# Optimization experiments

Hardware: AMD Instinct MI355X
Metric: run time of the kernel (lower is better)

The kernel has to match this reference:

```python
import jax, jax.numpy as jnp
import numpy as np
from jax import lax

B, CHI, CHO, H, W = 4, 256, 256, 96, 96
K = 9  # 3x3 kernel taps
BN_EPS = 1e-5


def setup_inputs() -> dict:
    key = jax.random.key(0)
    k1, k2, k3 = jax.random.split(key, 3)
    x = jax.random.normal(k1, (B, CHI, H, W), dtype=jnp.float32)
    # offset/mask conv: zero-init in DCNv2; use small random so sampling is exercised
    w_offset = jax.random.normal(k2, (3 * K, CHI, 3, 3), dtype=jnp.float32) * 0.01
    b_offset = jnp.zeros((3 * K,), dtype=jnp.float32)
    fan_in = CHI * K
    w_conv = jax.random.normal(k3, (CHO, CHI, 3, 3), dtype=jnp.float32) / np.sqrt(fan_in)
    b_conv = jnp.zeros((CHO,), dtype=jnp.float32)
    gamma = jnp.ones((CHO,), dtype=jnp.float32)
    beta = jnp.zeros((CHO,), dtype=jnp.float32)
    return {"x": x, "w_offset": w_offset, "b_offset": b_offset,
            "w_conv": w_conv, "b_conv": b_conv, "gamma": gamma, "beta": beta}


def _bilinear_gather(img, py, px):
    # img: [C, H, W]; py, px: [K, H, W] float sampling positions (zero padding)
    Hin, Win = img.shape[1], img.shape[2]
    y0 = jnp.floor(py)
    x0 = jnp.floor(px)
    ly = py - y0  # fractional parts (differentiable w.r.t. offsets)
    lx = px - x0
    y0i = y0.astype(jnp.int32)
    x0i = x0.astype(jnp.int32)

    def corner(yi, xi, wgt):
        valid = (yi >= 0) & (yi < Hin) & (xi >= 0) & (xi < Win)
        yc = jnp.clip(yi, 0, Hin - 1)
        xc = jnp.clip(xi, 0, Win - 1)
        v = img[:, yc, xc]  # [C, K, H, W]
        return v * (wgt * valid.astype(wgt.dtype))[None]

    return (corner(y0i, x0i, (1 - ly) * (1 - lx))
            + corner(y0i, x0i + 1, (1 - ly) * lx)
            + corner(y0i + 1, x0i, ly * (1 - lx))
            + corner(y0i + 1, x0i + 1, ly * lx))


def _forward(x, w_offset, b_offset, w_conv, b_conv, gamma, beta):
    # offset/mask branch: plain 3x3 conv, pad 1, stride 1
    om = lax.conv_general_dilated(
        x, w_offset, window_strides=(1, 1), padding=((1, 1), (1, 1)),
        dimension_numbers=("NCHW", "OIHW", "NCHW"))
    om = om + b_offset[None, :, None, None]            # [B, 27, H, W]
    dy = om[:, 0:2 * K:2]                              # [B, 9, H, W]
    dx = om[:, 1:2 * K:2]                              # [B, 9, H, W]
    mask = jax.nn.sigmoid(om[:, 2 * K:])               # [B, 9, H, W]

    # base sampling grid: p0 + pn  (stride 1, pad 1, dilation 1)
    ky, kx = jnp.meshgrid(jnp.arange(3), jnp.arange(3), indexing="ij")
    ky = ky.reshape(K).astype(x.dtype)
    kx = kx.reshape(K).astype(x.dtype)
    hh = jnp.arange(x.shape[2], dtype=x.dtype)
    ww = jnp.arange(x.shape[3], dtype=x.dtype)
    py = dy + (hh[None, :, None] + ky[:, None, None] - 1.0)[None]  # [B,9,H,W]
    px = dx + (ww[None, None, :] + kx[:, None, None] - 1.0)[None]  # [B,9,H,W]

    cols = jax.vmap(_bilinear_gather)(x, py, px)       # [B, C, 9, H, W]
    cols = cols * mask[:, None]                        # modulated (DCNv2)

    wk = w_conv.reshape(w_conv.shape[0], w_conv.shape[1], K)
    out = jnp.einsum("bckhw,ock->bohw", cols, wk) + b_conv[None, :, None, None]

    # BatchNorm2d (training mode: batch stats) + ReLU
    mu = out.mean(axis=(0, 2, 3))
    var = out.var(axis=(0, 2, 3))
    xh = (out - mu[None, :, None, None]) * lax.rsqrt(var + BN_EPS)[None, :, None, None]
    y = gamma[None, :, None, None] * xh + beta[None, :, None, None]
    return jax.nn.relu(y)


def reference(x, w_offset, b_offset, w_conv, b_conv, gamma, beta):
    return _forward(x, w_offset, b_offset, w_conv, b_conv, gamma, beta)
```

## Files before the change

### kernel.cpp

```cpp
#include <hip/hip_runtime.h>
#include <math.h>

#define BN_    4
#define CHI_   256
#define CHO_   256
#define HH_    96
#define WW_    96
#define HW_    (HH_*WW_)
#define KK_    9
#define CK_    (CHI_*KK_)
#define NRED_  (BN_*HW_)
#define BN_EPS_ 1e-5f


typedef short short8 __attribute__((ext_vector_type(8)));
typedef float f32x4  __attribute__((ext_vector_type(4)));

__device__ __forceinline__ unsigned short f2bf(float v) {
    union { float f; unsigned u; } c; c.f = v;
    unsigned lsb = (c.u >> 16) & 1u;
    c.u += 0x7fffu + lsb;
    return (unsigned short)(c.u >> 16);
}

__global__ __launch_bounds__(256) void w2b_perm(
    const float* __restrict__ w, unsigned short* __restrict__ wb)
{
    int idx = blockIdx.x * 256 + threadIdx.x;
    int o  = idx / CK_;
    int kk = idx - o * CK_;
    int k  = kk >> 8;
    int c  = kk & 255;
    wb[idx] = f2bf(w[o * CK_ + c * KK_ + k]);
}

__global__ __launch_bounds__(256) void w2b_perm27(
    const float* __restrict__ w, unsigned short* __restrict__ wb)
{
    int idx = blockIdx.x * 256 + threadIdx.x;
    int o  = idx / CK_;
    int kk = idx - o * CK_;
    int k  = kk >> 8;
    int c  = kk & 255;
    wb[idx] = f2bf(w[o * CK_ + c * KK_ + k]);
}

__global__ __launch_bounds__(256) void transpose_x(
    const float* __restrict__ x, float* __restrict__ xt)
{
    __shared__ float tile[64][65];
    const int t = threadIdx.x;
    const int bid = blockIdx.x;
    const int b  = bid / (144 * 4);
    const int r  = bid - b * 576;
    const int pt = r >> 2, ct = r & 3;
    const int p0 = pt * 64, c0 = ct * 64;

    const int px = t & 63, g = t >> 6;
#pragma unroll
    for (int i = 0; i < 16; i++) {
        int cr = g + i * 4;
        tile[cr][px] = x[((size_t)b * CHI_ + c0 + cr) * HW_ + p0 + px];
    }
    __syncthreads();
    const int c = t & 63;
#pragma unroll
    for (int i = 0; i < 16; i++) {
        int pr = g + i * 4;
        xt[((size_t)b * HW_ + p0 + pr) * CHI_ + c0 + c] = tile[c][pr];
    }
}

__global__ __launch_bounds__(256) void offset_nhwc(
    const float* __restrict__ xt, const unsigned short* __restrict__ wob,
    const float* __restrict__ bo, float* __restrict__ om)
{
    __shared__ __align__(16) unsigned short sW[32 * 64];
    __shared__ __align__(16) unsigned short sB[64 * 64];

    const int t = threadIdx.x;
    const int bid = blockIdx.x;
    const int u   = (bid & 7) * 72 + (bid >> 3);
    const int pixtile = u % 144;
    const int b       = u / 144;
    const int p0 = pixtile * 64;

    const int lane = t & 63, wave = t >> 6;
    const int quad = lane >> 4, l15 = lane & 15;
    const int pxl  = t >> 2;
    const int cg   = t & 3;
    const int aro  = t >> 3;
    const int ako  = t & 7;

    f32x4 acc[2];
    acc[0] = (f32x4){0.f,0.f,0.f,0.f};
    acc[1] = (f32x4){0.f,0.f,0.f,0.f};

    const float* xtb = xt + (size_t)b * HW_ * CHI_;
    char* sWb = (char*)sW;
    char* sBb = (char*)sB;

    const int p = p0 + pxl;
    const int h = p / WW_, w = p % WW_;

    for (int kc = 0; kc < 36; kc++) {
        if (kc) __syncthreads();
        {
            uint4 v = make_uint4(0u, 0u, 0u, 0u);
            if (aro < 27)
                v = *reinterpret_cast<const uint4*>(
                    wob + (size_t)aro * CK_ + kc * 64 + ako * 8);
            *reinterpret_cast<uint4*>(
                sWb + (aro << 7) + ((ako << 4) ^ ((aro & 7) << 4))) = v;
        }
        {
            const int k  = kc >> 2;
            const int c0 = (kc & 3) << 6;
            const int yy = h + k / 3 - 1;
            const int xx = w + (k % 3) - 1;
            const bool ok = ((unsigned)yy < HH_) & ((unsigned)xx < WW_);
            union { unsigned short s[16]; uint4 q[2]; } pk;
            if (ok) {
                const float4* src = reinterpret_cast<const float4*>(
                    xtb + (size_t)(yy * WW_ + xx) * CHI_ + c0 + cg * 16);
#pragma unroll
                for (int i = 0; i < 4; i++) {
                    float4 f = src[i];
                    pk.s[i * 4 + 0] = f2bf(f.x);
                    pk.s[i * 4 + 1] = f2bf(f.y);
                    pk.s[i * 4 + 2] = f2bf(f.z);
                    pk.s[i * 4 + 3] = f2bf(f.w);
                }
            } else {
                pk.q[0] = make_uint4(0u, 0u, 0u, 0u);
                pk.q[1] = make_uint4(0u, 0u, 0u, 0u);
            }
            const int u0 = cg << 1;
            *reinterpret_cast<uint4*>(
                sBb + (pxl << 7) + ((u0 << 4) ^ ((pxl & 7) << 4))) = pk.q[0];
            *reinterpret_cast<uint4*>(
                sBb + (pxl << 7) + (((u0 + 1) << 4) ^ ((pxl & 7) << 4))) = pk.q[1];
        }
        __syncthreads();
#pragma unroll
        for (int ks = 0; ks < 2; ks++) {
            short8 a0, a1, b0;
            {
                int r = l15;
                a0 = *reinterpret_cast<const short8*>(
                    sWb + (r << 7) + (((ks << 6) + (quad << 4)) ^ ((r & 7) << 4)));
                r = 16 + l15;
                a1 = *reinterpret_cast<const short8*>(
                    sWb + (r << 7) + (((ks << 6) + (quad << 4)) ^ ((r & 7) << 4)));
                r = wave * 16 + l15;
                b0 = *reinterpret_cast<const short8*>(
                    sBb + (r << 7) + (((ks << 6) + (quad << 4)) ^ ((r & 7) << 4)));
            }
            acc[0] = __builtin_amdgcn_mfma_f32_16x16x32_bf16(a0, b0, acc[0], 0, 0, 0);
            acc[1] = __builtin_amdgcn_mfma_f32_16x16x32_bf16(a1, b0, acc[1], 0, 0, 0);
        }
    }

#pragma unroll
    for (int mt = 0; mt < 2; mt++) {
#pragma unroll
        for (int r = 0; r < 4; r++) {
            int oc = mt * 16 + quad * 4 + r;
            if (oc < 27) {
                int pix = p0 + wave * 16 + l15;
                om[((size_t)b * 27 + oc) * HW_ + pix] = acc[mt][r] + bo[oc];
            }
        }
    }
}

__global__ __launch_bounds__(256, 4) void deform_fused(
    const float* __restrict__ xt, const float* __restrict__ om,
    const unsigned short* __restrict__ wb, const float* __restrict__ bconv,
    float* __restrict__ outb)
{
    __shared__ __align__(16) unsigned short sA[CHO_ * 64];
    __shared__ __align__(16) unsigned short sB[32 * 64];
    __shared__ float s_py[KK_ * 32], s_px[KK_ * 32], s_mask[KK_ * 32];

    const int t = threadIdx.x;
    const int bid = blockIdx.x;
    const int u   = (bid & 7) * 144 + (bid >> 3);
    const int pixtile = u % 288;
    const int b       = u / 288;
    const int p0 = pixtile * 32;

    for (int e = t; e < KK_ * 32; e += 256) {
        int k = e >> 5, i = e & 31;
        int p = p0 + i;
        int h = p / WW_, w = p % WW_;
        const float* omb = om + ((size_t)b * 27) * HW_ + p;
        float dy = omb[(2 * k) * HW_];
        float dx = omb[(2 * k + 1) * HW_];
        float m  = omb[(18 + k) * HW_];
        s_py[e]   = dy + (float)(h + k / 3 - 1);
        s_px[e]   = dx + (float)(w + (k % 3) - 1);
        s_mask[e] = 1.f / (1.f + __expf(-m));
    }

    const int lane = t & 63, wave = t >> 6;
    const int quad = lane >> 4, l15 = lane & 15;
    const int pxl  = t >> 3;
    const int cg   = t & 7;

    f32x4 acc[4][2];
#pragma unroll
    for (int m = 0; m < 4; m++)
#pragma unroll
        for (int n = 0; n < 2; n++)
            acc[m][n] = (f32x4){0.f, 0.f, 0.f, 0.f};

    const float* xtb = xt + (size_t)b * HW_ * CHI_;
    char* sAb = (char*)sA;
    char* sBb = (char*)sB;

    __syncthreads();

    for (int kc = 0; kc < 36; kc++) {
        const int j0 = kc * 64;
        if (kc) __syncthreads();
#pragma unroll
        for (int n = 0; n < 8; n++) {
            int e = t + n * 256;
            int ocl = e >> 3, ko = e & 7;
            uint4 v = *reinterpret_cast<const uint4*>(
                wb + (size_t)ocl * CK_ + j0 + ko * 8);
            *reinterpret_cast<uint4*>(
                sAb + (ocl << 7) + ((ko << 4) ^ ((ocl & 7) << 4))) = v;
        }
        {
            const int k  = kc >> 2;
            const int c0 = (kc & 3) << 6;
            const int e  = k * 32 + pxl;
            float py = s_py[e], pxx = s_px[e], msk = s_mask[e];
            float y0f = floorf(py), x0f = floorf(pxx);
            float ly = py - y0f, lx = pxx - x0f;
            int y0 = (int)y0f, x0 = (int)x0f;
            float vy0 = ((unsigned)y0       < HH_) ? 1.f : 0.f;
            float vy1 = ((unsigned)(y0 + 1) < HH_) ? 1.f : 0.f;
            float vx0 = ((unsigned)x0       < WW_) ? 1.f : 0.f;
            float vx1 = ((unsigned)(x0 + 1) < WW_) ? 1.f : 0.f;
            int yc0 = min(max(y0, 0), HH_ - 1), yc1 = min(max(y0 + 1, 0), HH_ - 1);
            int xc0 = min(max(x0, 0), WW_ - 1), xc1 = min(max(x0 + 1, 0), WW_ - 1);
            float wy0 = 1.f - ly, wx0 = 1.f - lx;
            float w00 = wy0 * wx0 * vy0 * vx0 * msk;
            float w01 = wy0 * lx  * vy0 * vx1 * msk;
            float w10 = ly  * wx0 * vy1 * vx0 * msk;
            float w11 = ly  * lx  * vy1 * vx1 * msk;
            const float* base = xtb + c0 + cg * 8;
            const float4* r00 = reinterpret_cast<const float4*>(
                base + (size_t)(yc0 * WW_ + xc0) * CHI_);
            const float4* r01 = reinterpret_cast<const float4*>(
                base + (size_t)(yc0 * WW_ + xc1) * CHI_);
            const float4* r10 = reinterpret_cast<const float4*>(
                base + (size_t)(yc1 * WW_ + xc0) * CHI_);
            const float4* r11 = reinterpret_cast<const float4*>(
                base + (size_t)(yc1 * WW_ + xc1) * CHI_);
            union { unsigned short s[8]; uint4 q; } pk;
#pragma unroll
            for (int i = 0; i < 2; i++) {
                float4 fa = r00[i], fb = r01[i], fc = r10[i], fd = r11[i];
                pk.s[i * 4 + 0] = f2bf(fa.x * w00 + fb.x * w01 + fc.x * w10 + fd.x * w11);
                pk.s[i * 4 + 1] = f2bf(fa.y * w00 + fb.y * w01 + fc.y * w10 + fd.y * w11);
                pk.s[i * 4 + 2] = f2bf(fa.z * w00 + fb.z * w01 + fc.z * w10 + fd.z * w11);
                pk.s[i * 4 + 3] = f2bf(fa.w * w00 + fb.w * w01 + fc.w * w10 + fd.w * w11);
            }
            *reinterpret_cast<uint4*>(
                sBb + (pxl << 7) + ((cg << 4) ^ ((pxl & 7) << 4))) = pk.q;
        }
        __syncthreads();
#pragma unroll
        for (int ks = 0; ks < 2; ks++) {
            short8 afr[4], bfr[2];
#pragma unroll
            for (int m = 0; m < 4; m++) {
                int r = wave * 64 + m * 16 + l15;
                afr[m] = *reinterpret_cast<const short8*>(
                    sAb + (r << 7) + (((ks << 6) + (quad << 4)) ^ ((r & 7) << 4)));
            }
#pragma unroll
            for (int n = 0; n < 2; n++) {
                int r = n * 16 + l15;
                bfr[n] = *reinterpret_cast<const short8*>(
                    sBb + (r << 7) + (((ks << 6) + (quad << 4)) ^ ((r & 7) << 4)));
            }
#pragma unroll
            for (int m = 0; m < 4; m++)
#pragma unroll
                for (int n = 0; n < 2; n++)
                    acc[m][n] = __builtin_amdgcn_mfma_f32_16x16x32_bf16(
                        afr[m], bfr[n], acc[m][n], 0, 0, 0);
        }
    }

#pragma unroll
    for (int m = 0; m < 4; m++) {
#pragma unroll
        for (int n = 0; n < 2; n++) {
#pragma unroll
            for (int r = 0; r < 4; r++) {
                int oc  = wave * 64 + m * 16 + quad * 4 + r;
                int pix = p0 + n * 16 + l15;
                outb[((size_t)b * CHO_ + oc) * HW_ + pix] = acc[m][n][r] + bconv[oc];
            }
        }
    }
}

__global__ __launch_bounds__(256) void bn_stats_part(
    const float* __restrict__ outb, float* __restrict__ part)
{
    const int bid = blockIdx.x;
    const int o = bid >> 3, sl = bid & 7;
    const int t = threadIdx.x;
    float s = 0.f, s2 = 0.f;
    for (int b = 0; b < BN_; b++) {
        const float4* base = reinterpret_cast<const float4*>(
            outb + ((size_t)b * CHO_ + o) * HW_ + sl * 1152);
        for (int i = t; i < 288; i += 256) {
            float4 v = base[i];
            s  += v.x + v.y + v.z + v.w;
            s2 += v.x * v.x + v.y * v.y + v.z * v.z + v.w * v.w;
        }
    }
#pragma unroll
    for (int off = 32; off > 0; off >>= 1) {
        s  += __shfl_down(s,  off, 64);
        s2 += __shfl_down(s2, off, 64);
    }
    __shared__ float rs[4], rs2[4];
    int lane = t & 63, wv = t >> 6;
    if (lane == 0) { rs[wv] = s; rs2[wv] = s2; }
    __syncthreads();
    if (t == 0) {
        part[o * 8 + sl]                = rs[0] + rs[1] + rs[2] + rs[3];
        part[CHO_ * 8 + o * 8 + sl]     = rs2[0] + rs2[1] + rs2[2] + rs2[3];
    }
}

__global__ __launch_bounds__(256) void bn_reduce(
    const float* __restrict__ part, float* __restrict__ stats)
{
    int o = threadIdx.x;
    float s = 0.f, s2 = 0.f;
#pragma unroll
    for (int i = 0; i < 8; i++) {
        s  += part[o * 8 + i];
        s2 += part[CHO_ * 8 + o * 8 + i];
    }
    stats[o]        = s;
    stats[CHO_ + o] = s2;
}

__global__ __launch_bounds__(256) void bn_apply(
    const float* __restrict__ outb, const float* __restrict__ stats,
    const float* __restrict__ gamma, const float* __restrict__ beta,
    float* __restrict__ y)
{
    unsigned idx = blockIdx.x * 256 + threadIdx.x;
    unsigned o = (idx / 2304u) & 255u;
    size_t i0 = (size_t)idx * 4;
    float4 v = *reinterpret_cast<const float4*>(outb + i0);
    const float invN = 1.f / (float)NRED_;
    float mu  = stats[o] * invN;
    float var = stats[CHO_ + o] * invN - mu * mu;
    float inv = rsqrtf(var + BN_EPS_);
    float sc = gamma[o] * inv;
    float sh = beta[o] - mu * sc;
    float4 r;
    r.x = fmaxf(v.x * sc + sh, 0.f);
    r.y = fmaxf(v.y * sc + sh, 0.f);
    r.z = fmaxf(v.z * sc + sh, 0.f);
    r.w = fmaxf(v.w * sc + sh, 0.f);
    *reinterpret_cast<float4*>(y + i0) = r;
}

extern "C" void kernel_launch(void* const* d_in, const int* in_sizes, int n_in,
                              void* d_out, int out_size, void* d_ws, size_t ws_size,
                              hipStream_t stream)
{
    const float* x   = (const float*)d_in[0];
    const float* wof = (const float*)d_in[1];
    const float* bof = (const float*)d_in[2];
    const float* wcv = (const float*)d_in[3];
    const float* bcv = (const float*)d_in[4];
    const float* gam = (const float*)d_in[5];
    const float* bet = (const float*)d_in[6];
    float* y = (float*)d_out;

    char* ws = (char*)d_ws;
    float*          om    = (float*)ws;
    float*          outb  = (float*)(ws + (size_t)4 * 1024 * 1024);
    float*          stats = (float*)(ws + (size_t)40 * 1024 * 1024);
    unsigned short* wbf2  = (unsigned short*)(ws + (size_t)40 * 1024 * 1024 + 8192);
    unsigned short* wob   = (unsigned short*)(ws + (size_t)40 * 1024 * 1024 + 8192 + 1179648);
    float*          xt    = (float*)(ws + (size_t)44 * 1024 * 1024);
    float*          part  = (float*)(ws + (size_t)82 * 1024 * 1024);

    w2b_perm<<<(CHO_ * CK_) / 256, 256, 0, stream>>>(wcv, wbf2);
    w2b_perm27<<<(27 * CK_) / 256, 256, 0, stream>>>(wof, wob);
    transpose_x<<<BN_ * 144 * 4, 256, 0, stream>>>(x, xt);
    offset_nhwc<<<BN_ * 144, 256, 0, stream>>>(xt, wob, bof, om);
    deform_fused<<<BN_ * 2 * (HW_ / 64), 256, 0, stream>>>(xt, om, wbf2, bcv, outb);
    bn_stats_part<<<CHO_ * 8, 256, 0, stream>>>(outb, part);
    bn_reduce<<<1, 256, 0, stream>>>(part, stats);
    bn_apply<<<(BN_ * CHO_ * HW_) / (4 * 256), 256, 0, stream>>>(outb, stats, gam, bet, y);
}
```

Before: 298.9 us.

## Precompute bf16 NHWC input and load deform weights via direct global-to-LDS

The transpose kernel now also writes a bf16 copy of the NHWC input, so the offset conv reads half the bytes and skips per-element float-to-bf16 conversion in its inner loop. In the fused deformable kernel, weight tiles are now loaded with global_load_lds straight into shared memory, with an XOR-swizzled source address that keeps the existing LDS swizzle layout. This removes the register round trip for the weight copy. The cost is an extra bf16 write pass in the transpose and a larger workspace.

Result: faster. 275.2 us (-7.9%).

```diff
diff --git a/kernel.cpp b/kernel.cpp
--- a/kernel.cpp
+++ b/kernel.cpp
@@ -46,7 +46,8 @@
 }
 
 __global__ __launch_bounds__(256) void transpose_x(
-    const float* __restrict__ x, float* __restrict__ xt)
+    const float* __restrict__ x, float* __restrict__ xt,
+    unsigned short* __restrict__ xt16)
 {
     __shared__ float tile[64][65];
     const int t = threadIdx.x;
@@ -67,12 +68,15 @@
 #pragma unroll
     for (int i = 0; i < 16; i++) {
         int pr = g + i * 4;
-        xt[((size_t)b * HW_ + p0 + pr) * CHI_ + c0 + c] = tile[c][pr];
+        float v = tile[c][pr];
+        size_t o = ((size_t)b * HW_ + p0 + pr) * CHI_ + c0 + c;
+        xt[o]   = v;
+        xt16[o] = f2bf(v);
     }
 }
 
 __global__ __launch_bounds__(256) void offset_nhwc(
-    const float* __restrict__ xt, const unsigned short* __restrict__ wob,
+    const unsigned short* __restrict__ xt16, const unsigned short* __restrict__ wob,
     const float* __restrict__ bo, float* __restrict__ om)
 {
     __shared__ __align__(16) unsigned short sW[32 * 64];
@@ -96,7 +100,7 @@
     acc[0] = (f32x4){0.f,0.f,0.f,0.f};
     acc[1] = (f32x4){0.f,0.f,0.f,0.f};
 
-    const float* xtb = xt + (size_t)b * HW_ * CHI_;
+    const unsigned short* xtb = xt16 + (size_t)b * HW_ * CHI_;
     char* sWb = (char*)sW;
     char* sBb = (char*)sB;
 
@@ -119,27 +123,19 @@
             const int yy = h + k / 3 - 1;
             const int xx = w + (k % 3) - 1;
             const bool ok = ((unsigned)yy < HH_) & ((unsigned)xx < WW_);
-            union { unsigned short s[16]; uint4 q[2]; } pk;
+            uint4 q0 = make_uint4(0u, 0u, 0u, 0u);
+            uint4 q1 = make_uint4(0u, 0u, 0u, 0u);
             if (ok) {
-                const float4* src = reinterpret_cast<const float4*>(
+                const uint4* src = reinterpret_cast<const uint4*>(
                     xtb + (size_t)(yy * WW_ + xx) * CHI_ + c0 + cg * 16);
-#pragma unroll
-                for (int i = 0; i < 4; i++) {
-                    float4 f = src[i];
-                    pk.s[i * 4 + 0] = f2bf(f.x);
-                    pk.s[i * 4 + 1] = f2bf(f.y);
-                    pk.s[i * 4 + 2] = f2bf(f.z);
-                    pk.s[i * 4 + 3] = f2bf(f.w);
-                }
-            } else {
-                pk.q[0] = make_uint4(0u, 0u, 0u, 0u);
-                pk.q[1] = make_uint4(0u, 0u, 0u, 0u);
+                q0 = src[0];
+                q1 = src[1];
             }
             const int u0 = cg << 1;
             *reinterpret_cast<uint4*>(
-                sBb + (pxl << 7) + ((u0 << 4) ^ ((pxl & 7) << 4))) = pk.q[0];
+                sBb + (pxl << 7) + ((u0 << 4) ^ ((pxl & 7) << 4))) = q0;
             *reinterpret_cast<uint4*>(
-                sBb + (pxl << 7) + (((u0 + 1) << 4) ^ ((pxl & 7) << 4))) = pk.q[1];
+                sBb + (pxl << 7) + (((u0 + 1) << 4) ^ ((pxl & 7) << 4))) = q1;
         }
         __syncthreads();
 #pragma unroll
@@ -207,6 +203,8 @@
     const int quad = lane >> 4, l15 = lane & 15;
     const int pxl  = t >> 3;
     const int cg   = t & 7;
+    const int lane8  = lane >> 3;
+    const int srcxor = ((lane & 7) ^ lane8) << 3;
 
     f32x4 acc[4][2];
 #pragma unroll
@@ -226,12 +224,13 @@
         if (kc) __syncthreads();
 #pragma unroll
         for (int n = 0; n < 8; n++) {
-            int e = t + n * 256;
-            int ocl = e >> 3, ko = e & 7;
-            uint4 v = *reinterpret_cast<const uint4*>(
-                wb + (size_t)ocl * CK_ + j0 + ko * 8);
-            *reinterpret_cast<uint4*>(
-                sAb + (ocl << 7) + ((ko << 4) ^ ((ocl & 7) << 4))) = v;
+            int base8 = n * 4 + wave;
+            int ocl   = base8 * 8 + lane8;
+            const unsigned short* g = wb + (size_t)ocl * CK_ + j0 + srcxor;
+            __builtin_amdgcn_global_load_lds(
+                (const __attribute__((address_space(1))) unsigned int*)g,
+                (__attribute__((address_space(3))) unsigned int*)(sAb + base8 * 1024),
+                16, 0, 0);
         }
         {
             const int k  = kc >> 2;
@@ -400,12 +399,13 @@
     unsigned short* wbf2  = (unsigned short*)(ws + (size_t)40 * 1024 * 1024 + 8192);
     unsigned short* wob   = (unsigned short*)(ws + (size_t)40 * 1024 * 1024 + 8192 + 1179648);
     float*          xt    = (float*)(ws + (size_t)44 * 1024 * 1024);
-    float*          part  = (float*)(ws + (size_t)82 * 1024 * 1024);
+    unsigned short* xt16  = (unsigned short*)(ws + (size_t)84 * 1024 * 1024);
+    float*          part  = (float*)(ws + (size_t)104 * 1024 * 1024);
 
     w2b_perm<<<(CHO_ * CK_) / 256, 256, 0, stream>>>(wcv, wbf2);
     w2b_perm27<<<(27 * CK_) / 256, 256, 0, stream>>>(wof, wob);
-    transpose_x<<<BN_ * 144 * 4, 256, 0, stream>>>(x, xt);
-    offset_nhwc<<<BN_ * 144, 256, 0, stream>>>(xt, wob, bof, om);
+    transpose_x<<<BN_ * 144 * 4, 256, 0, stream>>>(x, xt, xt16);
+    offset_nhwc<<<BN_ * 144, 256, 0, stream>>>(xt16, wob, bof, om);
     deform_fused<<<BN_ * 2 * (HW_ / 64), 256, 0, stream>>>(xt, om, wbf2, bcv, outb);
     bn_stats_part<<<CHO_ * 8, 256, 0, stream>>>(outb, part);
     bn_reduce<<<1, 256, 0, stream>>>(part, stats);
```
